# Kernel tuning notes

Measured on AMD Instinct MI355X. Metric: run time of the kernel, lower is better.

The kernel has to match this reference:

```python
import jax, jax.numpy as jnp
import numpy as np

V, H, HALF, B, L = 32000, 256, 128, 64, 512


def setup_inputs() -> dict:
    key = jax.random.key(0)
    ks = jax.random.split(key, 16)
    s = 0.02
    return {
        "seq": jax.random.randint(ks[0], (B, L), 0, V),
        "embed": jax.random.normal(ks[1], (V, H), jnp.float32) * s,
        "W1": jax.random.normal(ks[2], (H, 2 * H), jnp.float32) * s,
        "b1": jnp.zeros((2 * H,), jnp.float32),
        "W2": jax.random.normal(ks[3], (2 * H, H), jnp.float32) * s,
        "b2": jnp.zeros((H,), jnp.float32),
        "ln_g": jnp.ones((H,), jnp.float32),
        "ln_b": jnp.zeros((H,), jnp.float32),
        "Wsem": jax.random.normal(ks[4], (H, HALF), jnp.float32) * s,
        "bsem": jnp.zeros((HALF,), jnp.float32),
        "Wepi": jax.random.normal(ks[5], (H, HALF), jnp.float32) * s,
        "bepi": jnp.zeros((HALF,), jnp.float32),
        "Wout": jax.random.normal(ks[6], (2 * HALF, V), jnp.float32) * s,
        "bout": jnp.zeros((V,), jnp.float32),
    }


def _encode(seq, embed, W1, b1, W2, b2, ln_g, ln_b):
    e = embed[seq]                                  # [B, L, H]
    ff = jnp.maximum(e @ W1 + b1, 0.0) @ W2 + b2    # [B, L, H]
    x = e + ff
    mu = jnp.mean(x, -1, keepdims=True)
    var = jnp.mean((x - mu) ** 2, -1, keepdims=True)
    return (x - mu) / jnp.sqrt(var + 1e-5) * ln_g + ln_b


def _delta_step(carry, inp):
    M_s, M_e = carry
    ks, ke, scale = inp  # ks/ke: [B, half]; scale scalar
    vps = jnp.einsum("bij,bj->bi", M_s, ks)
    dvs = ks - vps / (jnp.sum(ks * ks, -1, keepdims=True) + 1e-6)
    M_s = M_s + dvs[:, :, None] * ks[:, None, :]
    vpe = jnp.einsum("bij,bj->bi", M_e, ke)
    dve = ke - vpe / (jnp.sum(ke * ke, -1, keepdims=True) + 1e-6)
    M_e = M_e + scale * (dve[:, :, None] * ke[:, None, :])
    return (M_s, M_e), None


def reference(seq, embed, W1, b1, W2, b2, ln_g, ln_b,
              Wsem, bsem, Wepi, bepi, Wout, bout):
    h = _encode(seq, embed, W1, b1, W2, b2, ln_g, ln_b)   # [B, L, H]
    Bs, Ls, _ = h.shape
    half = Wsem.shape[1]
    # keys for all write steps t = 0 .. L-2, precomputed in one GEMM
    ks_all = (h[:, :-1] @ Wsem + bsem).transpose(1, 0, 2)  # [L-1, B, half]
    ke_all = (h[:, :-1] @ Wepi + bepi).transpose(1, 0, 2)
    scales = jnp.arange(1, Ls, dtype=h.dtype) / Ls         # (t+1)/L
    M0 = jnp.zeros((Bs, half, half), h.dtype)
    (M_s, M_e), _ = jax.lax.scan(_delta_step, (M0, M0), (ks_all, ke_all, scales))
    q = h[:, -1, :]
    cs = jnp.einsum("bij,bj->bi", M_s, q @ Wsem + bsem)
    ce = jnp.einsum("bij,bj->bi", M_e, q @ Wepi + bepi)
    return jnp.concatenate([cs, ce], -1) @ Wout + bout     # [B, V]
```

## Files before the change

kernel.cpp:

```cpp
#include <hip/hip_runtime.h>
#include <hip/hip_bf16.h>
#include <stdint.h>

#define B_   64
#define L_   512
#define H_   256
#define H2_  512
#define HALF_ 128
#define V_   32000
#define NTOK_ (B_*L_)

typedef __attribute__((ext_vector_type(8))) short bf16x8;
typedef __attribute__((ext_vector_type(4))) float f32x4;

__device__ __forceinline__ float bf2f(short h){
    union { unsigned u; float f; } v; v.u = ((unsigned)(unsigned short)h) << 16; return v.f;
}
__device__ __forceinline__ short f2bf(float f){
    union { float f; unsigned u; } v; v.f = f;
    unsigned r = v.u + 0x7fffu + ((v.u >> 16) & 1u);
    return (short)(r >> 16);
}

__global__ __launch_bounds__(256) void k_prep(
    const float* __restrict__ W1, const float* __restrict__ W2,
    const float* __restrict__ Wsem, const float* __restrict__ Wepi,
    const float* __restrict__ bsem, const float* __restrict__ bepi,
    short* __restrict__ W1t, short* __restrict__ W2t, short* __restrict__ Wpt,
    float* __restrict__ bp)
{
    const int n = blockIdx.x, t = threadIdx.x;
    if (n < 512) {
        W1t[n*256 + t] = f2bf(W1[t*H2_ + n]);
    } else if (n < 768) {
        const int r = n - 512;
        W2t[r*512 + t]       = f2bf(W2[t*H_ + r]);
        W2t[r*512 + t + 256] = f2bf(W2[(t+256)*H_ + r]);
    } else {
        const int r = n - 768;
        Wpt[r*256 + t] = f2bf(r < 128 ? Wsem[t*HALF_ + r] : Wepi[t*HALF_ + (r-128)]);
        if (t == 0) bp[r] = (r < 128) ? bsem[r] : bepi[r-128];
    }
}

#define EA_LD 264

__global__ __launch_bounds__(512, 4) void k_encode_fused(
    const int* __restrict__ seq, const float* __restrict__ embed,
    const short* __restrict__ W1t, const float* __restrict__ b1,
    const short* __restrict__ W2t, const float* __restrict__ b2,
    const float* __restrict__ ln_g, const float* __restrict__ ln_b,
    const short* __restrict__ Wpt, const float* __restrict__ bp,
    float* __restrict__ kske)
{
    __shared__ __align__(16) short eA[64*EA_LD];
    __shared__ __align__(16) short fB[64*EA_LD];
    __shared__ float2 lnp[8][64];
    __shared__ float2 stat[64];

    const int tid = threadIdx.x;
    const int lo  = tid & 15;
    const int hi  = (tid >> 4) & 3;
    const int wv  = tid >> 6;
    const int n0  = wv * 32;
    const int tokBase = blockIdx.x * 64;
    short* hA = eA;

    {
        const int tk = tid >> 3, part = tid & 7;
        const float4* src = (const float4*)(embed + (size_t)seq[tokBase + tk] * H_);
#pragma unroll
        for (int i = 0; i < 8; ++i) {
            float4 v = src[part + 8*i];
            short4 o; o.x = f2bf(v.x); o.y = f2bf(v.y); o.z = f2bf(v.z); o.w = f2bf(v.w);
            *(short4*)&eA[tk*EA_LD + (part + 8*i)*4] = o;
        }
    }
    __syncthreads();

    f32x4 acc2[4][2];
#pragma unroll
    for (int m = 0; m < 4; ++m) { acc2[m][0] = (f32x4){0,0,0,0}; acc2[m][1] = (f32x4){0,0,0,0}; }

    for (int h = 0; h < 2; ++h) {
        f32x4 acc1[4][2];
#pragma unroll
        for (int m = 0; m < 4; ++m) { acc1[m][0] = (f32x4){0,0,0,0}; acc1[m][1] = (f32x4){0,0,0,0}; }
        {
            const short* Bb = W1t + ((size_t)(h*256 + n0 + lo))*256;
            bf16x8 bc0 = *(const bf16x8*)(Bb + 8*hi);
            bf16x8 bc1 = *(const bf16x8*)(Bb + 16*256 + 8*hi);
#pragma unroll
            for (int kk = 0; kk < 8; ++kk) {
                const int k0 = kk*32 + 8*hi;
                bf16x8 bn0, bn1;
                if (kk < 7) {
                    bn0 = *(const bf16x8*)(Bb + k0 + 32);
                    bn1 = *(const bf16x8*)(Bb + 16*256 + k0 + 32);
                }
#pragma unroll
                for (int m = 0; m < 4; ++m) {
                    bf16x8 a = *(const bf16x8*)&eA[(lo + 16*m)*EA_LD + k0];
                    acc1[m][0] = __builtin_amdgcn_mfma_f32_16x16x32_bf16(a, bc0, acc1[m][0], 0,0,0);
                    acc1[m][1] = __builtin_amdgcn_mfma_f32_16x16x32_bf16(a, bc1, acc1[m][1], 0,0,0);
                }
                if (kk < 7) { bc0 = bn0; bc1 = bn1; }
            }
        }
        {
            const float bb0 = b1[h*256 + n0 + lo];
            const float bb1 = b1[h*256 + n0 + 16 + lo];
#pragma unroll
            for (int m = 0; m < 4; ++m)
#pragma unroll
                for (int r = 0; r < 4; ++r) {
                    const int row = m*16 + hi*4 + r;
                    fB[row*EA_LD + n0 + lo]      = f2bf(fmaxf(acc1[m][0][r] + bb0, 0.f));
                    fB[row*EA_LD + n0 + 16 + lo] = f2bf(fmaxf(acc1[m][1][r] + bb1, 0.f));
                }
        }
        __syncthreads();
        {
            const short* Bb = W2t + ((size_t)(n0 + lo))*512 + h*256;
            bf16x8 bc0 = *(const bf16x8*)(Bb + 8*hi);
            bf16x8 bc1 = *(const bf16x8*)(Bb + 16*512 + 8*hi);
#pragma unroll
            for (int kk = 0; kk < 8; ++kk) {
                const int k0 = kk*32 + 8*hi;
                bf16x8 bn0, bn1;
                if (kk < 7) {
                    bn0 = *(const bf16x8*)(Bb + k0 + 32);
                    bn1 = *(const bf16x8*)(Bb + 16*512 + k0 + 32);
                }
#pragma unroll
                for (int m = 0; m < 4; ++m) {
                    bf16x8 a = *(const bf16x8*)&fB[(lo + 16*m)*EA_LD + k0];
                    acc2[m][0] = __builtin_amdgcn_mfma_f32_16x16x32_bf16(a, bc0, acc2[m][0], 0,0,0);
                    acc2[m][1] = __builtin_amdgcn_mfma_f32_16x16x32_bf16(a, bc1, acc2[m][1], 0,0,0);
                }
                if (kk < 7) { bc0 = bn0; bc1 = bn1; }
            }
        }
        __syncthreads();
    }

    const int col0 = n0 + lo, col1 = n0 + 16 + lo;

    {
        const float bb0 = b2[col0], bb1 = b2[col1];
#pragma unroll
        for (int m = 0; m < 4; ++m)
#pragma unroll
            for (int r = 0; r < 4; ++r) {
                const int row = m*16 + hi*4 + r;
                acc2[m][0][r] += bb0 + bf2f(eA[row*EA_LD + col0]);
                acc2[m][1][r] += bb1 + bf2f(eA[row*EA_LD + col1]);
            }
#pragma unroll
        for (int m = 0; m < 4; ++m)
#pragma unroll
            for (int r = 0; r < 4; ++r) {
                float x0 = acc2[m][0][r], x1 = acc2[m][1][r];
                float s  = x0 + x1;
                float s2 = fmaf(x0, x0, x1*x1);
#pragma unroll
                for (int o = 1; o < 16; o <<= 1) { s += __shfl_xor(s, o, 64); s2 += __shfl_xor(s2, o, 64); }
                if (lo == 0) { float2 p; p.x = s; p.y = s2; lnp[wv][m*16 + hi*4 + r] = p; }
            }
    }
    __syncthreads();
    if (tid < 64) {
        float s = 0.f, s2 = 0.f;
#pragma unroll
        for (int w = 0; w < 8; ++w) { float2 p = lnp[w][tid]; s += p.x; s2 += p.y; }
        float mu  = s * (1.f/256.f);
        float var = s2 * (1.f/256.f) - mu*mu;
        float2 st; st.x = mu; st.y = rsqrtf(var + 1e-5f);
        stat[tid] = st;
    }
    __syncthreads();

    {
        const float g0 = ln_g[col0], g1 = ln_g[col1];
        const float be0 = ln_b[col0], be1 = ln_b[col1];
#pragma unroll
        for (int m = 0; m < 4; ++m)
#pragma unroll
            for (int r = 0; r < 4; ++r) {
                const int row = m*16 + hi*4 + r;
                float2 st = stat[row];
                hA[row*EA_LD + col0] = f2bf((acc2[m][0][r] - st.x) * st.y * g0 + be0);
                hA[row*EA_LD + col1] = f2bf((acc2[m][1][r] - st.x) * st.y * g1 + be1);
            }
    }
    __syncthreads();

    f32x4 acc3[4][2];
#pragma unroll
    for (int m = 0; m < 4; ++m) { acc3[m][0] = (f32x4){0,0,0,0}; acc3[m][1] = (f32x4){0,0,0,0}; }
    {
        const short* Bb = Wpt + ((size_t)(n0 + lo))*256;
        bf16x8 bc0 = *(const bf16x8*)(Bb + 8*hi);
        bf16x8 bc1 = *(const bf16x8*)(Bb + 16*256 + 8*hi);
#pragma unroll
        for (int kk = 0; kk < 8; ++kk) {
            const int k0 = kk*32 + 8*hi;
            bf16x8 bn0, bn1;
            if (kk < 7) {
                bn0 = *(const bf16x8*)(Bb + k0 + 32);
                bn1 = *(const bf16x8*)(Bb + 16*256 + k0 + 32);
            }
#pragma unroll
            for (int m = 0; m < 4; ++m) {
                bf16x8 a = *(const bf16x8*)&hA[(lo + 16*m)*EA_LD + k0];
                acc3[m][0] = __builtin_amdgcn_mfma_f32_16x16x32_bf16(a, bc0, acc3[m][0], 0,0,0);
                acc3[m][1] = __builtin_amdgcn_mfma_f32_16x16x32_bf16(a, bc1, acc3[m][1], 0,0,0);
            }
            if (kk < 7) { bc0 = bn0; bc1 = bn1; }
        }
    }
    {
        const float bp0 = bp[col0], bp1 = bp[col1];
#pragma unroll
        for (int m = 0; m < 4; ++m)
#pragma unroll
            for (int r = 0; r < 4; ++r) {
                const int row = m*16 + hi*4 + r;
                kske[(size_t)(tokBase + row)*256 + col0] = acc3[m][0][r] + bp0;
                kske[(size_t)(tokBase + row)*256 + col1] = acc3[m][1][r] + bp1;
            }
    }
}

#define SCAN_BODY(CC, GA, KXA, KYA, NGA, GB, KXB, KYB, NGB) do {              \
    const int c_ = (CC);                                                      \
    wls[2*l] = w.x; wls[2*l+1] = w.y;                                         \
    float p0=0.f, p1=0.f, p2=0.f, p3=0.f;                                     \
    _Pragma("unroll")                                                         \
    for (int i = 0; i < 8; ++i) {                                             \
        float4 wv2 = *(const float4*)&wls[q*32 + 4*i];                        \
        p0 = fmaf(kq[i].x, wv2.x, p0); p1 = fmaf(kq[i].y, wv2.y, p1);         \
        p2 = fmaf(kq[i].z, wv2.z, p2); p3 = fmaf(kq[i].w, wv2.w, p3);         \
    }                                                                         \
    float bb = (p0 + p1) + (p2 + p3);                                         \
    bb += __shfl_xor(bb, 16, 64);                                             \
    bb += __shfl_xor(bb, 32, 64);                                             \
    if (c_ > 0) {                                                             \
        const float* krow = kb + ((size_t)((c_-1)*16 + lo))*256 + q*32;       \
        _Pragma("unroll")                                                     \
        for (int i = 0; i < 8; ++i) kq[i] = *(const float4*)(krow + 4*i);     \
        const float* gr = &Gs[(c_-1)*256 + lo*16];                            \
        _Pragma("unroll")                                                     \
        for (int i = 0; i < 4; ++i) {                                         \
            float4 gt = *(const float4*)(gr + 4*i);                           \
            GB[4*i]=gt.x; GB[4*i+1]=gt.y; GB[4*i+2]=gt.z; GB[4*i+3]=gt.w;     \
        }                                                                     \
        NGB = gvs[(c_-1)*16 + lo];                                            \
        const float* kdr = kb + ((size_t)((c_-1)*16))*256 + 2*l;              \
        _Pragma("unroll")                                                     \
        for (int j = 0; j < 16; ++j) {                                        \
            float2 kt = *(const float2*)(kdr + (size_t)j*256);                \
            KXB[j] = kt.x; KYB[j] = kt.y;                                     \
        }                                                                     \
    }                                                                         \
    const int tl_ = c_*16 + lo;                                               \
    const float cl_ = chain ? ((tl_ < 511) ? (float)(tl_+1)*(1.f/512.f) : 0.f)\
                            : ((tl_ < 511) ? 1.f : 0.f);                      \
    _Pragma("unroll")                                                         \
    for (int j = 15; j >= 0; --j) {                                           \
        float dj = __int_as_float(__builtin_amdgcn_readlane(__float_as_int(bb), j)); \
        bb = fmaf(dj, GA[j], bb);                                             \
        float tg = NGA * dj;                                                  \
        float tc = cl_ * dj;                                                  \
        float gd = __int_as_float(__builtin_amdgcn_readlane(__float_as_int(tg), j)); \
        float cd = __int_as_float(__builtin_amdgcn_readlane(__float_as_int(tc), j)); \
        w.x = fmaf(gd, KXA[j], w.x);  w.y = fmaf(gd, KYA[j], w.y);            \
        ax  = fmaf(cd, KXA[j], ax);   ay  = fmaf(cd, KYA[j], ay);             \
    }                                                                         \
} while (0)

__global__ __launch_bounds__(256) void k_scan(
    const float* __restrict__ kske, short* __restrict__ chi, short* __restrict__ clo)
{
    __shared__ float Gs[32*256];
    __shared__ float gvs[32*16];
    __shared__ float wls[128];

    const int b = blockIdx.x, chain = blockIdx.y;
    const int tid = threadIdx.x;
    const int wvi = tid >> 6;
    const int l   = tid & 63;
    const int lo  = l & 15, q = l >> 4;
    const float* kb = kske + ((size_t)b*L_)*256 + chain*HALF_;

    for (int cc = 0; cc < 8; ++cc) {
        const int c = wvi*8 + cc;
        const float* rowp = kb + ((size_t)(c*16 + lo))*256 + 8*q;
        bf16x8 ah[4], al[4];
#pragma unroll
        for (int m = 0; m < 4; ++m) {
            float4 v0 = *(const float4*)(rowp + m*32);
            float4 v1 = *(const float4*)(rowp + m*32 + 4);
            float f[8] = {v0.x,v0.y,v0.z,v0.w,v1.x,v1.y,v1.z,v1.w};
#pragma unroll
            for (int i = 0; i < 8; ++i) {
                short hh = f2bf(f[i]);
                ah[m][i] = hh;
                al[m][i] = f2bf(f[i] - bf2f(hh));
            }
        }
        f32x4 g = {0.f,0.f,0.f,0.f};
#pragma unroll
        for (int m = 0; m < 4; ++m) {
            g = __builtin_amdgcn_mfma_f32_16x16x32_bf16(ah[m], ah[m], g, 0,0,0);
            g = __builtin_amdgcn_mfma_f32_16x16x32_bf16(ah[m], al[m], g, 0,0,0);
            g = __builtin_amdgcn_mfma_f32_16x16x32_bf16(al[m], ah[m], g, 0,0,0);
        }
        float cand = (lo & 2) ? ((lo & 1) ? g[3] : g[2]) : ((lo & 1) ? g[1] : g[0]);
        float dval = __shfl(cand, (lo >> 2)*16 + lo, 64);

        const int tcol = c*16 + lo;
        float beta = 1.f / (dval + 1e-6f);
        float gam  = chain ? ((float)(tcol+1) * (1.f/512.f)) * beta : beta;
        if (tcol == 511) gam = 0.f;
#pragma unroll
        for (int r = 0; r < 4; ++r)
            Gs[c*256 + (4*q + r)*16 + lo] = -gam * g[r];
        if (l < 16) gvs[c*16 + lo] = -gam;
    }
    __syncthreads();
    if (wvi != 0) return;

    float2 w = *(const float2*)(kb + (size_t)511*256 + 2*l);
    float ax = 0.f, ay = 0.f;

    float ga[16], kxa[16], kya[16], nga;
    float gb_[16], kxb[16], kyb[16], ngb;
    float4 kq[8];

    {
        const float* krow = kb + ((size_t)(31*16 + lo))*256 + q*32;
#pragma unroll
        for (int i = 0; i < 8; ++i) kq[i] = *(const float4*)(krow + 4*i);
        const float* gr = &Gs[31*256 + lo*16];
#pragma unroll
        for (int i = 0; i < 4; ++i) {
            float4 gt = *(const float4*)(gr + 4*i);
            ga[4*i]=gt.x; ga[4*i+1]=gt.y; ga[4*i+2]=gt.z; ga[4*i+3]=gt.w;
        }
        nga = gvs[31*16 + lo];
        const float* kdr = kb + ((size_t)(31*16))*256 + 2*l;
#pragma unroll
        for (int j = 0; j < 16; ++j) {
            float2 kt = *(const float2*)(kdr + (size_t)j*256);
            kxa[j] = kt.x; kya[j] = kt.y;
        }
    }

    for (int it = 0; it < 16; ++it) {
        SCAN_BODY(31 - 2*it, ga,  kxa, kya, nga, gb_, kxb, kyb, ngb);
        SCAN_BODY(30 - 2*it, gb_, kxb, kyb, ngb, ga,  kxa, kya, nga);
    }

    short2 hv, lv;
    hv.x = f2bf(ax); lv.x = f2bf(ax - bf2f(hv.x));
    hv.y = f2bf(ay); lv.y = f2bf(ay - bf2f(hv.y));
    *(short2*)&chi[b*256 + chain*HALF_ + 2*l] = hv;
    *(short2*)&clo[b*256 + chain*HALF_ + 2*l] = lv;
}

__global__ __launch_bounds__(256) void k_out(
    const short* __restrict__ chi, const short* __restrict__ clo,
    const float* __restrict__ Wout, const float* __restrict__ bout,
    float* __restrict__ out)
{
    __shared__ __align__(16) short ch_s[64*EA_LD];
    __shared__ __align__(16) short cl_s[64*EA_LD];
    const int t  = threadIdx.x;
    const int lo = t & 15;
    const int hi = (t >> 4) & 3;
    const int wv = t >> 6;

    {
        const int4* sh = (const int4*)chi;
        const int4* sl = (const int4*)clo;
#pragma unroll
        for (int i = 0; i < 8; ++i) {
            const int idx = t + 256*i;
            const int row = idx >> 5;
            const int c8  = (idx & 31) * 8;
            *(int4*)&ch_s[row*EA_LD + c8] = sh[idx];
            *(int4*)&cl_s[row*EA_LD + c8] = sl[idx];
        }
    }
    __syncthreads();

    const int colbase = blockIdx.x * 64 + wv * 16;
    f32x4 acc[4];
#pragma unroll
    for (int m = 0; m < 4; ++m) acc[m] = (f32x4){0.f,0.f,0.f,0.f};

#pragma unroll
    for (int kk = 0; kk < 8; ++kk) {
        const int k0 = kk*32 + 8*hi;
        bf16x8 bh, bl;
#pragma unroll
        for (int i = 0; i < 8; ++i) {
            float wf = Wout[(size_t)(k0 + i)*V_ + colbase + lo];
            short wh = f2bf(wf);
            bh[i] = wh;
            bl[i] = f2bf(wf - bf2f(wh));
        }
#pragma unroll
        for (int m = 0; m < 4; ++m) {
            bf16x8 ah = *(const bf16x8*)&ch_s[(m*16 + lo)*EA_LD + k0];
            bf16x8 al = *(const bf16x8*)&cl_s[(m*16 + lo)*EA_LD + k0];
            acc[m] = __builtin_amdgcn_mfma_f32_16x16x32_bf16(ah, bh, acc[m], 0,0,0);
            acc[m] = __builtin_amdgcn_mfma_f32_16x16x32_bf16(ah, bl, acc[m], 0,0,0);
            acc[m] = __builtin_amdgcn_mfma_f32_16x16x32_bf16(al, bh, acc[m], 0,0,0);
        }
    }

    const float bo = bout[colbase + lo];
#pragma unroll
    for (int m = 0; m < 4; ++m)
#pragma unroll
        for (int r = 0; r < 4; ++r)
            out[(size_t)(m*16 + hi*4 + r)*V_ + colbase + lo] = acc[m][r] + bo;
}

extern "C" void kernel_launch(void* const* d_in, const int* in_sizes, int n_in,
                              void* d_out, int out_size, void* d_ws, size_t ws_size,
                              hipStream_t stream)
{
    (void)in_sizes; (void)n_in; (void)out_size; (void)ws_size;
    const int*   seq   = (const int*)  d_in[0];
    const float* embed = (const float*)d_in[1];
    const float* W1    = (const float*)d_in[2];
    const float* b1    = (const float*)d_in[3];
    const float* W2    = (const float*)d_in[4];
    const float* b2    = (const float*)d_in[5];
    const float* ln_g  = (const float*)d_in[6];
    const float* ln_b  = (const float*)d_in[7];
    const float* Wsem  = (const float*)d_in[8];
    const float* bsem  = (const float*)d_in[9];
    const float* Wepi  = (const float*)d_in[10];
    const float* bepi  = (const float*)d_in[11];
    const float* Wout  = (const float*)d_in[12];
    const float* bout  = (const float*)d_in[13];
    float* out = (float*)d_out;

    char* wp = (char*)d_ws;
    short* W1t = (short*)wp;  wp += (size_t)512*256*2;
    short* W2t = (short*)wp;  wp += (size_t)256*512*2;
    short* Wpt = (short*)wp;  wp += (size_t)256*256*2;
    float* bp  = (float*)wp;  wp += 256*4;
    float* kske= (float*)wp;  wp += (size_t)NTOK_*256*4;
    short* chi = (short*)wp;  wp += (size_t)B_*256*2;
    short* clo = (short*)wp;  wp += (size_t)B_*256*2;

    k_prep<<<1024, 256, 0, stream>>>(W1, W2, Wsem, Wepi, bsem, bepi, W1t, W2t, Wpt, bp);
    k_encode_fused<<<NTOK_/64, 512, 0, stream>>>(seq, embed, W1t, b1, W2t, b2,
                                                 ln_g, ln_b, Wpt, bp, kske);
    k_scan<<<dim3(B_, 2), 256, 0, stream>>>(kske, chi, clo);
    k_out<<<V_/64, 256, 0, stream>>>(chi, clo, Wout, bout, out);
}
```

Before: 104.0 us.

## Merge prep into encode and scan into output via atomic-ticket grid barriers

Folds the weight transpose/convert kernel into the encoder kernel, and the scan kernel into the output GEMM kernel. Blocks first pull work tickets from a global atomic counter and then spin-wait on a completion counter before starting the dependent phase. This removes two kernel launches and their inter-kernel gaps, and it adds a memset for the counters. The spin-wait assumes that every block which took a ticket makes progress, so it relies on enough co-resident blocks to avoid deadlock. Early blocks also busy-wait while the scan and prep work finishes.

Result: slower. 323.7 us (+211.1%).

```diff
diff --git a/kernel.cpp b/kernel.cpp
--- a/kernel.cpp
+++ b/kernel.cpp
@@ -22,43 +22,64 @@
     return (short)(r >> 16);
 }
 
-__global__ __launch_bounds__(256) void k_prep(
-    const float* __restrict__ W1, const float* __restrict__ W2,
-    const float* __restrict__ Wsem, const float* __restrict__ Wepi,
-    const float* __restrict__ bsem, const float* __restrict__ bepi,
+#define EA_LD 264
+#define PREP_TICKETS 641u
+#define SCAN_TICKETS 128u
+
+__global__ __launch_bounds__(512, 4) void k_prep_encode(
+    const int* __restrict__ seq, const float* __restrict__ embed,
+    const float* __restrict__ W1, const float* __restrict__ b1,
+    const float* __restrict__ W2, const float* __restrict__ b2,
+    const float* __restrict__ ln_g, const float* __restrict__ ln_b,
+    const float* __restrict__ Wsem, const float* __restrict__ bsem,
+    const float* __restrict__ Wepi, const float* __restrict__ bepi,
+    unsigned* __restrict__ ctr,
     short* __restrict__ W1t, short* __restrict__ W2t, short* __restrict__ Wpt,
-    float* __restrict__ bp)
-{
-    const int n = blockIdx.x, t = threadIdx.x;
-    if (n < 512) {
-        W1t[n*256 + t] = f2bf(W1[t*H2_ + n]);
-    } else if (n < 768) {
-        const int r = n - 512;
-        W2t[r*512 + t]       = f2bf(W2[t*H_ + r]);
-        W2t[r*512 + t + 256] = f2bf(W2[(t+256)*H_ + r]);
-    } else {
-        const int r = n - 768;
-        Wpt[r*256 + t] = f2bf(r < 128 ? Wsem[t*HALF_ + r] : Wepi[t*HALF_ + (r-128)]);
-        if (t == 0) bp[r] = (r < 128) ? bsem[r] : bepi[r-128];
-    }
-}
-
-#define EA_LD 264
-
-__global__ __launch_bounds__(512, 4) void k_encode_fused(
-    const int* __restrict__ seq, const float* __restrict__ embed,
-    const short* __restrict__ W1t, const float* __restrict__ b1,
-    const short* __restrict__ W2t, const float* __restrict__ b2,
-    const float* __restrict__ ln_g, const float* __restrict__ ln_b,
-    const short* __restrict__ Wpt, const float* __restrict__ bp,
-    float* __restrict__ kske)
+    float* __restrict__ bp, float* __restrict__ kske)
 {
     __shared__ __align__(16) short eA[64*EA_LD];
     __shared__ __align__(16) short fB[64*EA_LD];
     __shared__ float2 lnp[8][64];
     __shared__ float2 stat[64];
+    __shared__ unsigned sT;
 
     const int tid = threadIdx.x;
+
+    unsigned items = 0;
+    for (;;) {
+        __syncthreads();
+        if (tid == 0) sT = atomicAdd(&ctr[0], 1u);
+        __syncthreads();
+        const unsigned t = sT;
+        if (t >= PREP_TICKETS) break;
+        const unsigned idx = t * 512u + (unsigned)tid;
+        if (idx < 131072u) {
+            unsigned k = idx >> 9, n = idx & 511u;
+            W1t[n*256u + k] = f2bf(W1[k*512u + n]);
+        } else if (idx < 262144u) {
+            unsigned j = idx - 131072u;
+            unsigned k = j >> 8, n = j & 255u;
+            W2t[n*512u + k] = f2bf(W2[k*256u + n]);
+        } else if (idx < 327680u) {
+            unsigned j = idx - 262144u;
+            unsigned k = j >> 8, n = j & 255u;
+            float a = (n < 128u) ? Wsem[k*HALF_ + n] : Wepi[k*HALF_ + (n-128u)];
+            Wpt[n*256u + k] = f2bf(a);
+        } else if (idx < 327936u) {
+            unsigned c = idx - 327680u;
+            bp[c] = (c < 128u) ? bsem[c] : bepi[c-128u];
+        }
+        ++items;
+    }
+    __threadfence();
+    __syncthreads();
+    if (tid == 0 && items) atomicAdd(&ctr[1], items);
+    if (tid == 0) {
+        while (atomicAdd(&ctr[1], 0u) < PREP_TICKETS) __builtin_amdgcn_s_sleep(8);
+    }
+    __syncthreads();
+    __threadfence();
+
     const int lo  = tid & 15;
     const int hi  = (tid >> 4) & 3;
     const int wv  = tid >> 6;
@@ -279,114 +300,131 @@
     }                                                                         \
 } while (0)
 
-__global__ __launch_bounds__(256) void k_scan(
-    const float* __restrict__ kske, short* __restrict__ chi, short* __restrict__ clo)
+__global__ __launch_bounds__(256) void k_scan_out(
+    const float* __restrict__ kske, unsigned* __restrict__ ctr,
+    short* __restrict__ chi, short* __restrict__ clo,
+    const float* __restrict__ Wout, const float* __restrict__ bout,
+    float* __restrict__ out)
 {
-    __shared__ float Gs[32*256];
-    __shared__ float gvs[32*16];
-    __shared__ float wls[128];
-
-    const int b = blockIdx.x, chain = blockIdx.y;
+    __shared__ __align__(16) char smem2[67584];
+    float* Gs   = (float*)smem2;
+    float* gvs  = (float*)(smem2 + 32768);
+    float* wls  = (float*)(smem2 + 34816);
+    short* ch_s = (short*)smem2;
+    short* cl_s = (short*)(smem2 + 33792);
+    __shared__ unsigned sT;
+
     const int tid = threadIdx.x;
     const int wvi = tid >> 6;
     const int l   = tid & 63;
-    const int lo  = l & 15, q = l >> 4;
-    const float* kb = kske + ((size_t)b*L_)*256 + chain*HALF_;
-
-    for (int cc = 0; cc < 8; ++cc) {
-        const int c = wvi*8 + cc;
-        const float* rowp = kb + ((size_t)(c*16 + lo))*256 + 8*q;
-        bf16x8 ah[4], al[4];
-#pragma unroll
-        for (int m = 0; m < 4; ++m) {
-            float4 v0 = *(const float4*)(rowp + m*32);
-            float4 v1 = *(const float4*)(rowp + m*32 + 4);
-            float f[8] = {v0.x,v0.y,v0.z,v0.w,v1.x,v1.y,v1.z,v1.w};
-#pragma unroll
-            for (int i = 0; i < 8; ++i) {
-                short hh = f2bf(f[i]);
-                ah[m][i] = hh;
-                al[m][i] = f2bf(f[i] - bf2f(hh));
-            }
-        }
-        f32x4 g = {0.f,0.f,0.f,0.f};
-#pragma unroll
-        for (int m = 0; m < 4; ++m) {
-            g = __builtin_amdgcn_mfma_f32_16x16x32_bf16(ah[m], ah[m], g, 0,0,0);
-            g = __builtin_amdgcn_mfma_f32_16x16x32_bf16(ah[m], al[m], g, 0,0,0);
-            g = __builtin_amdgcn_mfma_f32_16x16x32_bf16(al[m], ah[m], g, 0,0,0);
-        }
-        float cand = (lo & 2) ? ((lo & 1) ? g[3] : g[2]) : ((lo & 1) ? g[1] : g[0]);
-        float dval = __shfl(cand, (lo >> 2)*16 + lo, 64);
-
-        const int tcol = c*16 + lo;
-        float beta = 1.f / (dval + 1e-6f);
-        float gam  = chain ? ((float)(tcol+1) * (1.f/512.f)) * beta : beta;
-        if (tcol == 511) gam = 0.f;
-#pragma unroll
-        for (int r = 0; r < 4; ++r)
-            Gs[c*256 + (4*q + r)*16 + lo] = -gam * g[r];
-        if (l < 16) gvs[c*16 + lo] = -gam;
-    }
-    __syncthreads();
-    if (wvi != 0) return;
-
-    float2 w = *(const float2*)(kb + (size_t)511*256 + 2*l);
-    float ax = 0.f, ay = 0.f;
-
-    float ga[16], kxa[16], kya[16], nga;
-    float gb_[16], kxb[16], kyb[16], ngb;
-    float4 kq[8];
-
-    {
-        const float* krow = kb + ((size_t)(31*16 + lo))*256 + q*32;
-#pragma unroll
-        for (int i = 0; i < 8; ++i) kq[i] = *(const float4*)(krow + 4*i);
-        const float* gr = &Gs[31*256 + lo*16];
-#pragma unroll
-        for (int i = 0; i < 4; ++i) {
-            float4 gt = *(const float4*)(gr + 4*i);
-            ga[4*i]=gt.x; ga[4*i+1]=gt.y; ga[4*i+2]=gt.z; ga[4*i+3]=gt.w;
-        }
-        nga = gvs[31*16 + lo];
-        const float* kdr = kb + ((size_t)(31*16))*256 + 2*l;
-#pragma unroll
-        for (int j = 0; j < 16; ++j) {
-            float2 kt = *(const float2*)(kdr + (size_t)j*256);
-            kxa[j] = kt.x; kya[j] = kt.y;
-        }
-    }
-
-    for (int it = 0; it < 16; ++it) {
-        SCAN_BODY(31 - 2*it, ga,  kxa, kya, nga, gb_, kxb, kyb, ngb);
-        SCAN_BODY(30 - 2*it, gb_, kxb, kyb, ngb, ga,  kxa, kya, nga);
-    }
-
-    short2 hv, lv;
-    hv.x = f2bf(ax); lv.x = f2bf(ax - bf2f(hv.x));
-    hv.y = f2bf(ay); lv.y = f2bf(ay - bf2f(hv.y));
-    *(short2*)&chi[b*256 + chain*HALF_ + 2*l] = hv;
-    *(short2*)&clo[b*256 + chain*HALF_ + 2*l] = lv;
-}
-
-__global__ __launch_bounds__(256) void k_out(
-    const short* __restrict__ chi, const short* __restrict__ clo,
-    const float* __restrict__ Wout, const float* __restrict__ bout,
-    float* __restrict__ out)
-{
-    __shared__ __align__(16) short ch_s[64*EA_LD];
-    __shared__ __align__(16) short cl_s[64*EA_LD];
-    const int t  = threadIdx.x;
-    const int lo = t & 15;
-    const int hi = (t >> 4) & 3;
-    const int wv = t >> 6;
+    const int slo = l & 15, q = l >> 4;
+
+    for (;;) {
+        __syncthreads();
+        if (tid == 0) sT = atomicAdd(&ctr[2], 1u);
+        __syncthreads();
+        const unsigned t = sT;
+        if (t >= SCAN_TICKETS) break;
+        const int b = (int)(t >> 1), chain = (int)(t & 1u);
+        const int lo = slo;
+        const float* kb = kske + ((size_t)b*L_)*256 + chain*HALF_;
+
+        for (int cc = 0; cc < 8; ++cc) {
+            const int c = wvi*8 + cc;
+            const float* rowp = kb + ((size_t)(c*16 + lo))*256 + 8*q;
+            bf16x8 ah[4], al[4];
+#pragma unroll
+            for (int m = 0; m < 4; ++m) {
+                float4 v0 = *(const float4*)(rowp + m*32);
+                float4 v1 = *(const float4*)(rowp + m*32 + 4);
+                float f[8] = {v0.x,v0.y,v0.z,v0.w,v1.x,v1.y,v1.z,v1.w};
+#pragma unroll
+                for (int i = 0; i < 8; ++i) {
+                    short hh = f2bf(f[i]);
+                    ah[m][i] = hh;
+                    al[m][i] = f2bf(f[i] - bf2f(hh));
+                }
+            }
+            f32x4 g = {0.f,0.f,0.f,0.f};
+#pragma unroll
+            for (int m = 0; m < 4; ++m) {
+                g = __builtin_amdgcn_mfma_f32_16x16x32_bf16(ah[m], ah[m], g, 0,0,0);
+                g = __builtin_amdgcn_mfma_f32_16x16x32_bf16(ah[m], al[m], g, 0,0,0);
+                g = __builtin_amdgcn_mfma_f32_16x16x32_bf16(al[m], ah[m], g, 0,0,0);
+            }
+            float cand = (lo & 2) ? ((lo & 1) ? g[3] : g[2]) : ((lo & 1) ? g[1] : g[0]);
+            float dval = __shfl(cand, (lo >> 2)*16 + lo, 64);
+
+            const int tcol = c*16 + lo;
+            float beta = 1.f / (dval + 1e-6f);
+            float gam  = chain ? ((float)(tcol+1) * (1.f/512.f)) * beta : beta;
+            if (tcol == 511) gam = 0.f;
+#pragma unroll
+            for (int r = 0; r < 4; ++r)
+                Gs[c*256 + (4*q + r)*16 + lo] = -gam * g[r];
+            if (l < 16) gvs[c*16 + lo] = -gam;
+        }
+        __syncthreads();
+
+        if (wvi == 0) {
+            float2 w = *(const float2*)(kb + (size_t)511*256 + 2*l);
+            float ax = 0.f, ay = 0.f;
+
+            float ga[16], kxa[16], kya[16], nga;
+            float gb_[16], kxb[16], kyb[16], ngb;
+            float4 kq[8];
+
+            {
+                const float* krow = kb + ((size_t)(31*16 + lo))*256 + q*32;
+#pragma unroll
+                for (int i = 0; i < 8; ++i) kq[i] = *(const float4*)(krow + 4*i);
+                const float* gr = &Gs[31*256 + lo*16];
+#pragma unroll
+                for (int i = 0; i < 4; ++i) {
+                    float4 gt = *(const float4*)(gr + 4*i);
+                    ga[4*i]=gt.x; ga[4*i+1]=gt.y; ga[4*i+2]=gt.z; ga[4*i+3]=gt.w;
+                }
+                nga = gvs[31*16 + lo];
+                const float* kdr = kb + ((size_t)(31*16))*256 + 2*l;
+#pragma unroll
+                for (int j = 0; j < 16; ++j) {
+                    float2 kt = *(const float2*)(kdr + (size_t)j*256);
+                    kxa[j] = kt.x; kya[j] = kt.y;
+                }
+            }
+
+            for (int it = 0; it < 16; ++it) {
+                SCAN_BODY(31 - 2*it, ga,  kxa, kya, nga, gb_, kxb, kyb, ngb);
+                SCAN_BODY(30 - 2*it, gb_, kxb, kyb, ngb, ga,  kxa, kya, nga);
+            }
+
+            short2 hv, lv;
+            hv.x = f2bf(ax); lv.x = f2bf(ax - bf2f(hv.x));
+            hv.y = f2bf(ay); lv.y = f2bf(ay - bf2f(hv.y));
+            *(short2*)&chi[b*256 + chain*HALF_ + 2*l] = hv;
+            *(short2*)&clo[b*256 + chain*HALF_ + 2*l] = lv;
+        }
+        __threadfence();
+        __syncthreads();
+        if (tid == 0) atomicAdd(&ctr[3], 1u);
+    }
+
+    if (tid == 0) {
+        while (atomicAdd(&ctr[3], 0u) < SCAN_TICKETS) __builtin_amdgcn_s_sleep(8);
+    }
+    __syncthreads();
+    __threadfence();
+
+    const int lo = tid & 15;
+    const int hi = (tid >> 4) & 3;
+    const int wv = tid >> 6;
 
     {
         const int4* sh = (const int4*)chi;
         const int4* sl = (const int4*)clo;
 #pragma unroll
         for (int i = 0; i < 8; ++i) {
-            const int idx = t + 256*i;
+            const int idx = tid + 256*i;
             const int row = idx >> 5;
             const int c8  = (idx & 31) * 8;
             *(int4*)&ch_s[row*EA_LD + c8] = sh[idx];
@@ -451,6 +489,7 @@
     float* out = (float*)d_out;
 
     char* wp = (char*)d_ws;
+    unsigned* ctr = (unsigned*)wp;  wp += 256;
     short* W1t = (short*)wp;  wp += (size_t)512*256*2;
     short* W2t = (short*)wp;  wp += (size_t)256*512*2;
     short* Wpt = (short*)wp;  wp += (size_t)256*256*2;
@@ -459,9 +498,9 @@
     short* chi = (short*)wp;  wp += (size_t)B_*256*2;
     short* clo = (short*)wp;  wp += (size_t)B_*256*2;
 
-    k_prep<<<1024, 256, 0, stream>>>(W1, W2, Wsem, Wepi, bsem, bepi, W1t, W2t, Wpt, bp);
-    k_encode_fused<<<NTOK_/64, 512, 0, stream>>>(seq, embed, W1t, b1, W2t, b2,
-                                                 ln_g, ln_b, Wpt, bp, kske);
-    k_scan<<<dim3(B_, 2), 256, 0, stream>>>(kske, chi, clo);
-    k_out<<<V_/64, 256, 0, stream>>>(chi, clo, Wout, bout, out);
+    hipMemsetAsync(ctr, 0, 256, stream);
+    k_prep_encode<<<NTOK_/64, 512, 0, stream>>>(seq, embed, W1, b1, W2, b2,
+                                                ln_g, ln_b, Wsem, bsem, Wepi, bepi,
+                                                ctr, W1t, W2t, Wpt, bp, kske);
+    k_scan_out<<<V_/64, 256, 0, stream>>>(kske, ctr, chi, clo, Wout, bout, out);
 }
```
